# Kernel optimization log

Hardware: AMD Instinct MI355X
Metric: run time of the kernel (lower is better)

Reference implementation:

```python
import jax, jax.numpy as jnp
import numpy as np

NUM_HEADS = 8
IN_DIM = 384
HEAD_DIM = IN_DIM // NUM_HEADS  # 48


def setup_inputs() -> dict:
    key = jax.random.key(0)
    ks = jax.random.split(key, 6)
    B, N, M, C = 4, 4096, 1024, 384
    q_x = jax.random.normal(ks[0], (B, N, C), dtype=jnp.float32)
    kv_x = jax.random.normal(ks[1], (B, M, C), dtype=jnp.float32)
    s = C ** -0.5  # fan-in style init scale
    Wq = jax.random.normal(ks[2], (C, IN_DIM), dtype=jnp.float32) * s
    Wkv = jax.random.normal(ks[3], (C, 2 * IN_DIM), dtype=jnp.float32) * s
    Wproj = jax.random.normal(ks[4], (IN_DIM, IN_DIM), dtype=jnp.float32) * (IN_DIM ** -0.5)
    bproj = jnp.zeros((IN_DIM,), dtype=jnp.float32)
    return {"q_x": q_x, "kv_x": kv_x, "Wq": Wq, "Wkv": Wkv, "Wproj": Wproj, "bproj": bproj}


def reference(q_x, kv_x, Wq, Wkv, Wproj, bproj):
    B, N, C = q_x.shape
    M = kv_x.shape[1]
    scale = HEAD_DIM ** -0.5
    # q: [B, H, N, hd]
    q = (q_x @ Wq).reshape(B, N, NUM_HEADS, HEAD_DIM).transpose(0, 2, 1, 3)
    # k, v: [B, H, M, hd]
    kv = (kv_x @ Wkv).reshape(B, M, 2, NUM_HEADS, HEAD_DIM).transpose(2, 0, 3, 1, 4)
    k, v = kv[0], kv[1]
    # attention scores [B, H, N, M]
    attn = jax.nn.softmax(jnp.einsum('bhnd,bhmd->bhnm', q, k) * scale, axis=-1)
    x = jnp.einsum('bhnm,bhmd->bhnd', attn, v)  # [B, H, N, hd]
    x = x.transpose(0, 2, 1, 3).reshape(B, N, IN_DIM)
    x = x @ Wproj + bproj
    # sr_ratio == 1 residual: add raw q projection back
    q_res = q.transpose(0, 2, 1, 3).reshape(B, N, IN_DIM)
    return q_res + x
```

## Files before the change

### kernel.cpp

```cpp
#include <hip/hip_runtime.h>
#include <hip/hip_bf16.h>
#include <math.h>

#define B_ 4
#define N_ 4096
#define M_ 1024
#define C_ 384
#define NH_ 8
#define HD_ 48

typedef float f32x4 __attribute__((ext_vector_type(4)));
typedef short bf16x8 __attribute__((ext_vector_type(8)));

__device__ __forceinline__ unsigned short f2bf(float x) {
    unsigned int u = __builtin_bit_cast(unsigned int, x);
    return (unsigned short)((u + 0x7FFFu + ((u >> 16) & 1u)) >> 16);
}
__device__ __forceinline__ unsigned short f2bf_trunc(float x) {
    return (unsigned short)(__builtin_bit_cast(unsigned int, x) >> 16);
}
__device__ __forceinline__ float fast_exp2(float x) {
#if __has_builtin(__builtin_amdgcn_exp2f)
    return __builtin_amdgcn_exp2f(x);
#else
    return exp2f(x);
#endif
}

#define QSCALE 0.20823490983597203f

__global__ __launch_bounds__(256)
void conv_act(const float* __restrict__ a, unsigned short* __restrict__ da,
              const float* __restrict__ b, unsigned short* __restrict__ db)
{
    size_t i4 = (size_t)blockIdx.x * 256 + threadIdx.x;
    const float* src; unsigned short* dst;
    if (i4 < 1572864u) { src = a; dst = da; }
    else { src = b; dst = db; i4 -= 1572864u; }
    float4 v = *(const float4*)&src[i4 * 4];
    uint2 pk;
    pk.x = (unsigned int)f2bf(v.x) | ((unsigned int)f2bf(v.y) << 16);
    pk.y = (unsigned int)f2bf(v.z) | ((unsigned int)f2bf(v.w) << 16);
    *(uint2*)&dst[i4 * 4] = pk;
}

__global__ __launch_bounds__(256)
void transpose_w3(const float* __restrict__ Wq, const float* __restrict__ Wkv,
                  const float* __restrict__ Wproj,
                  unsigned short* __restrict__ Wq_t, unsigned short* __restrict__ Wkv_t,
                  unsigned short* __restrict__ Wproj_t)
{
    __shared__ unsigned short T[64 * 72];
    const int tid = threadIdx.x;
    int bid = blockIdx.x;
    const float* W; unsigned short* Wt; int N, kt, nt;
    if (bid < 36)       { W = Wq;    Wt = Wq_t;    N = 384; kt = bid / 6;  nt = bid - kt * 6; }
    else if (bid < 108) { bid -= 36;  W = Wkv;   Wt = Wkv_t;   N = 768; kt = bid / 12; nt = bid - kt * 12; }
    else                { bid -= 108; W = Wproj; Wt = Wproj_t; N = 384; kt = bid / 6;  nt = bid - kt * 6; }
    const int k0 = kt * 64, n0 = nt * 64;

    #pragma unroll
    for (int it = 0; it < 4; ++it) {
        int k = it * 16 + (tid >> 4);
        int n4 = (tid & 15) * 4;
        float4 v = *(const float4*)&W[(size_t)(k0 + k) * N + n0 + n4];
        T[(n4 + 0) * 72 + k] = f2bf(v.x);
        T[(n4 + 1) * 72 + k] = f2bf(v.y);
        T[(n4 + 2) * 72 + k] = f2bf(v.z);
        T[(n4 + 3) * 72 + k] = f2bf(v.w);
    }
    __syncthreads();
    #pragma unroll
    for (int i = 0; i < 2; ++i) {
        int s = tid + 256 * i;
        int n = s >> 3, part = s & 7;
        *(uint4*)&Wt[(size_t)(n0 + n) * C_ + k0 + part * 8] = *(const uint4*)&T[n * 72 + part * 8];
    }
}

__global__ __launch_bounds__(256)
void gemm_bf16(const unsigned short* __restrict__ A, const unsigned short* __restrict__ Wt,
               float* __restrict__ out0,
               unsigned short* __restrict__ bf0, unsigned short* __restrict__ bf1,
               const float* __restrict__ addend, const float* __restrict__ bias,
               int mode)
{
    __shared__ unsigned short As[128 * 72];
    __shared__ unsigned short Ws[64 * 72];
    const int tid = threadIdx.x;
    const int wave = tid >> 6;
    const int lane = tid & 63;
    const int ln = lane & 15;
    const int quad = lane >> 4;
    const int row0 = blockIdx.x * 128;
    const int col0 = blockIdx.y * 64;

    f32x4 acc[2][4];
    #pragma unroll
    for (int rt = 0; rt < 2; ++rt)
        #pragma unroll
        for (int t = 0; t < 4; ++t) acc[rt][t] = (f32x4){0.f, 0.f, 0.f, 0.f};

    for (int kk = 0; kk < C_; kk += 64) {
        __syncthreads();
        #pragma unroll
        for (int i = 0; i < 4; ++i) {
            int s = tid + 256 * i;
            int r = s >> 3, part = s & 7;
            *(uint4*)&As[r * 72 + part * 8] =
                *(const uint4*)&A[(size_t)(row0 + r) * C_ + kk + part * 8];
        }
        #pragma unroll
        for (int i = 0; i < 2; ++i) {
            int s = tid + 256 * i;
            int n = s >> 3, part = s & 7;
            *(uint4*)&Ws[n * 72 + part * 8] =
                *(const uint4*)&Wt[(size_t)(col0 + n) * C_ + kk + part * 8];
        }
        __syncthreads();

        bf16x8 af[2][2];
        #pragma unroll
        for (int rt = 0; rt < 2; ++rt) {
            const unsigned short* Ap = &As[(wave * 32 + rt * 16 + ln) * 72];
            af[rt][0] = *(const bf16x8*)&Ap[quad * 8];
            af[rt][1] = *(const bf16x8*)&Ap[32 + quad * 8];
        }
        #pragma unroll
        for (int t = 0; t < 4; ++t) {
            const unsigned short* Wp = &Ws[(t * 16 + ln) * 72];
            bf16x8 b0 = *(const bf16x8*)&Wp[quad * 8];
            bf16x8 b1 = *(const bf16x8*)&Wp[32 + quad * 8];
            #pragma unroll
            for (int rt = 0; rt < 2; ++rt) {
                acc[rt][t] = __builtin_amdgcn_mfma_f32_16x16x32_bf16(af[rt][0], b0, acc[rt][t], 0, 0, 0);
                acc[rt][t] = __builtin_amdgcn_mfma_f32_16x16x32_bf16(af[rt][1], b1, acc[rt][t], 0, 0, 0);
            }
        }
    }

    #pragma unroll
    for (int rt = 0; rt < 2; ++rt) {
        #pragma unroll
        for (int t = 0; t < 4; ++t) {
            int gcol = col0 + t * 16 + ln;
            #pragma unroll
            for (int r = 0; r < 4; ++r) {
                int grow = row0 + wave * 32 + rt * 16 + quad * 4 + r;
                float v = acc[rt][t][r];
                if (mode == 0) {
                    out0[(size_t)grow * C_ + gcol] = v;
                    int b = grow >> 12, n = grow & (N_ - 1);
                    int h = gcol / HD_, d = gcol - h * HD_;
                    bf0[(((size_t)(b * NH_ + h) * N_) + n) * HD_ + d] = f2bf(v * QSCALE);
                } else if (mode == 1) {
                    int b = grow >> 10, m = grow & (M_ - 1);
                    if (gcol < C_) {
                        int h = gcol / HD_, d = gcol - h * HD_;
                        bf0[(((size_t)(b * NH_ + h) * M_) + m) * HD_ + d] = f2bf(v);
                    } else {
                        int c2 = gcol - C_;
                        int h = c2 / HD_, d = c2 - h * HD_;
                        bf1[(((size_t)(b * NH_ + h) * HD_) + d) * M_ + m] = f2bf(v);
                    }
                } else {
                    size_t idx = (size_t)grow * C_ + gcol;
                    out0[idx] = v + addend[idx] + bias[gcol];
                }
            }
        }
    }
}

__global__ __launch_bounds__(256)
void attn_mfma(const unsigned short* __restrict__ qbf,
               const unsigned short* __restrict__ kbf,
               const unsigned short* __restrict__ vbf,
               unsigned short* __restrict__ of)
{
    __shared__ unsigned short QP[64 * 72];
    __shared__ unsigned short Ks[64 * 72];
    __shared__ unsigned short Vt[64 * 72];

    const int tid = threadIdx.x;
    const int wave = tid >> 6;
    const int lane = tid & 63;
    const int ln = lane & 15;
    const int quad = lane >> 4;
    const int bh = blockIdx.y;
    const int n0 = blockIdx.x * 64;

    uint4 z4; z4.x = z4.y = z4.z = z4.w = 0u;
    for (int e = tid; e < 576; e += 256) {
        *(uint4*)&QP[e * 8] = z4;
        *(uint4*)&Ks[e * 8] = z4;
        *(uint4*)&Vt[e * 8] = z4;
    }
    __syncthreads();
    if (tid < 64) Vt[48 * 72 + tid] = 0x3F80;
    const unsigned short* qsrc = qbf + ((size_t)bh * N_ + n0) * HD_;
    for (int e = tid; e < 384; e += 256) {
        int r = e / 6, part = e - r * 6;
        *(uint4*)&QP[r * 72 + part * 8] = *(const uint4*)&qsrc[r * HD_ + part * 8];
    }
    __syncthreads();

    const unsigned short* Qw = &QP[(wave * 16 + ln) * 72];
    bf16x8 aq0 = *(const bf16x8*)&Qw[quad * 8];
    bf16x8 aq1 = *(const bf16x8*)&Qw[32 + quad * 8];

    f32x4 O[4];
    #pragma unroll
    for (int t = 0; t < 4; ++t) O[t] = (f32x4){0.f, 0.f, 0.f, 0.f};

    const unsigned short* ksrc = kbf + (size_t)bh * M_ * HD_;
    const unsigned short* vsrc = vbf + (size_t)bh * HD_ * M_;
    unsigned short* Pw = &QP[wave * 16 * 72];
    const int phys_r = (ln & 3) * 4 + (ln >> 2);
    const unsigned short* Pr = &QP[(wave * 16 + phys_r) * 72];

    for (int mt = 0; mt < M_ / 64; ++mt) {
        __syncthreads();
        const unsigned short* kp = ksrc + (size_t)mt * 64 * HD_;
        for (int e = tid; e < 384; e += 256) {
            int r = e / 6, part = e - r * 6;
            *(uint4*)&Ks[r * 72 + part * 8] = *(const uint4*)&kp[r * HD_ + part * 8];
        }
        for (int e = tid; e < 384; e += 256) {
            int d = e >> 3, part = e & 7;
            *(uint4*)&Vt[d * 72 + part * 8] =
                *(const uint4*)&vsrc[(size_t)d * M_ + mt * 64 + part * 8];
        }
        __syncthreads();

        f32x4 S[4];
        #pragma unroll
        for (int t = 0; t < 4; ++t) S[t] = (f32x4){0.f, 0.f, 0.f, 0.f};
        #pragma unroll
        for (int t = 0; t < 4; ++t) {
            const unsigned short* Kp = &Ks[(t * 16 + ln) * 72];
            bf16x8 b0 = *(const bf16x8*)&Kp[quad * 8];
            S[t] = __builtin_amdgcn_mfma_f32_16x16x32_bf16(aq0, b0, S[t], 0, 0, 0);
            bf16x8 b1 = *(const bf16x8*)&Kp[32 + quad * 8];
            S[t] = __builtin_amdgcn_mfma_f32_16x16x32_bf16(aq1, b1, S[t], 0, 0, 0);
        }

        #pragma unroll
        for (int t = 0; t < 4; ++t)
            #pragma unroll
            for (int r = 0; r < 4; ++r)
                Pw[(r * 4 + quad) * 72 + t * 16 + ln] = f2bf_trunc(fast_exp2(S[t][r]));

        bf16x8 pa0 = *(const bf16x8*)&Pr[quad * 8];
        bf16x8 pa1 = *(const bf16x8*)&Pr[32 + quad * 8];
        #pragma unroll
        for (int ot = 0; ot < 4; ++ot) {
            const unsigned short* Vp = &Vt[(ot * 16 + ln) * 72];
            bf16x8 b0 = *(const bf16x8*)&Vp[quad * 8];
            O[ot] = __builtin_amdgcn_mfma_f32_16x16x32_bf16(pa0, b0, O[ot], 0, 0, 0);
            bf16x8 b1 = *(const bf16x8*)&Vp[32 + quad * 8];
            O[ot] = __builtin_amdgcn_mfma_f32_16x16x32_bf16(pa1, b1, O[ot], 0, 0, 0);
        }
    }

    const int b = bh >> 3, h = bh & 7;
    float inv[4];
    #pragma unroll
    for (int r = 0; r < 4; ++r)
        inv[r] = 1.0f / __shfl(O[3][r], lane & 48);
    #pragma unroll
    for (int ot = 0; ot < 3; ++ot) {
        int gcol = h * HD_ + ot * 16 + ln;
        #pragma unroll
        for (int r = 0; r < 4; ++r) {
            int grow = n0 + wave * 16 + quad * 4 + r;
            of[((size_t)b * N_ + grow) * C_ + gcol] = f2bf(O[ot][r] * inv[r]);
        }
    }
}

extern "C" void kernel_launch(void* const* d_in, const int* in_sizes, int n_in,
                              void* d_out, int out_size, void* d_ws, size_t ws_size,
                              hipStream_t stream) {
    const float* q_x   = (const float*)d_in[0];
    const float* kv_x  = (const float*)d_in[1];
    const float* Wq    = (const float*)d_in[2];
    const float* Wkv   = (const float*)d_in[3];
    const float* Wproj = (const float*)d_in[4];
    const float* bproj = (const float*)d_in[5];
    float* out = (float*)d_out;

    float* qf = (float*)d_ws;
    unsigned short* base = (unsigned short*)(qf + 6291456);
    unsigned short* qx_bf   = base;
    unsigned short* kvx_bf  = qx_bf  + 6291456;
    unsigned short* qbf     = kvx_bf + 1572864;
    unsigned short* kbf     = qbf    + 6291456;
    unsigned short* vbf     = kbf    + 1572864;
    unsigned short* Wq_t    = vbf    + 1572864;
    unsigned short* Wkv_t   = Wq_t   + 147456;
    unsigned short* Wproj_t = Wkv_t  + 294912;
    unsigned short* of      = qx_bf;

    dim3 blk(256);

    conv_act<<<dim3(7680), blk, 0, stream>>>(q_x, qx_bf, kv_x, kvx_bf);
    transpose_w3<<<dim3(144), blk, 0, stream>>>(Wq, Wkv, Wproj, Wq_t, Wkv_t, Wproj_t);

    gemm_bf16<<<dim3(128, 6), blk, 0, stream>>>(
        qx_bf, Wq_t, qf, qbf, nullptr, nullptr, nullptr, 0);

    gemm_bf16<<<dim3(32, 12), blk, 0, stream>>>(
        kvx_bf, Wkv_t, nullptr, kbf, vbf, nullptr, nullptr, 1);

    attn_mfma<<<dim3(64, 32), blk, 0, stream>>>(qbf, kbf, vbf, of);

    gemm_bf16<<<dim3(128, 6), blk, 0, stream>>>(
        of, Wproj_t, out, nullptr, nullptr, qf, bproj, 2);
}
```

Baseline: 208.4 us.

## Fuse activation conversion into GEMMs and restructure attention without LDS K/V staging

Removes the separate fp32-to-bf16 conversion kernel by converting activations inside the GEMM A-tile load, and stores the q residual as bf16 instead of fp32 to cut bandwidth. The attention kernel is rewritten so each wave handles 32 query rows, loading K and V fragments directly from global memory instead of staging them in shared memory with block barriers, and computing the softmax denominator via an MFMA against a ones vector. This trades barrier and LDS traffic for redundant global/L2 reads per wave and adds bf16 rounding of the residual.

```diff
diff --git a/kernel.cpp b/kernel.cpp
--- a/kernel.cpp
+++ b/kernel.cpp
@@ -19,6 +19,9 @@
 __device__ __forceinline__ unsigned short f2bf_trunc(float x) {
     return (unsigned short)(__builtin_bit_cast(unsigned int, x) >> 16);
 }
+__device__ __forceinline__ float bf2f(unsigned short x) {
+    return __builtin_bit_cast(float, (unsigned int)x << 16);
+}
 __device__ __forceinline__ float fast_exp2(float x) {
 #if __has_builtin(__builtin_amdgcn_exp2f)
     return __builtin_amdgcn_exp2f(x);
@@ -28,21 +31,6 @@
 }
 
 #define QSCALE 0.20823490983597203f
-
-__global__ __launch_bounds__(256)
-void conv_act(const float* __restrict__ a, unsigned short* __restrict__ da,
-              const float* __restrict__ b, unsigned short* __restrict__ db)
-{
-    size_t i4 = (size_t)blockIdx.x * 256 + threadIdx.x;
-    const float* src; unsigned short* dst;
-    if (i4 < 1572864u) { src = a; dst = da; }
-    else { src = b; dst = db; i4 -= 1572864u; }
-    float4 v = *(const float4*)&src[i4 * 4];
-    uint2 pk;
-    pk.x = (unsigned int)f2bf(v.x) | ((unsigned int)f2bf(v.y) << 16);
-    pk.y = (unsigned int)f2bf(v.z) | ((unsigned int)f2bf(v.w) << 16);
-    *(uint2*)&dst[i4 * 4] = pk;
-}
 
 __global__ __launch_bounds__(256)
 void transpose_w3(const float* __restrict__ Wq, const float* __restrict__ Wkv,
@@ -79,11 +67,11 @@
 }
 
 __global__ __launch_bounds__(256)
-void gemm_bf16(const unsigned short* __restrict__ A, const unsigned short* __restrict__ Wt,
+void gemm_bf16(const void* __restrict__ Av, const unsigned short* __restrict__ Wt,
                float* __restrict__ out0,
                unsigned short* __restrict__ bf0, unsigned short* __restrict__ bf1,
-               const float* __restrict__ addend, const float* __restrict__ bias,
-               int mode)
+               const unsigned short* __restrict__ addend, const float* __restrict__ bias,
+               int mode, int a_bf16)
 {
     __shared__ unsigned short As[128 * 72];
     __shared__ unsigned short Ws[64 * 72];
@@ -103,12 +91,27 @@
 
     for (int kk = 0; kk < C_; kk += 64) {
         __syncthreads();
-        #pragma unroll
-        for (int i = 0; i < 4; ++i) {
-            int s = tid + 256 * i;
-            int r = s >> 3, part = s & 7;
-            *(uint4*)&As[r * 72 + part * 8] =
-                *(const uint4*)&A[(size_t)(row0 + r) * C_ + kk + part * 8];
+        if (a_bf16) {
+            const unsigned short* A = (const unsigned short*)Av;
+            #pragma unroll
+            for (int i = 0; i < 4; ++i) {
+                int s = tid + 256 * i;
+                int r = s >> 3, part = s & 7;
+                *(uint4*)&As[r * 72 + part * 8] =
+                    *(const uint4*)&A[(size_t)(row0 + r) * C_ + kk + part * 8];
+            }
+        } else {
+            const float* A = (const float*)Av;
+            #pragma unroll
+            for (int i = 0; i < 8; ++i) {
+                int s = tid + 256 * i;
+                int r = s >> 4, k4 = (s & 15) << 2;
+                float4 v = *(const float4*)&A[(size_t)(row0 + r) * C_ + kk + k4];
+                uint2 pk;
+                pk.x = (unsigned int)f2bf(v.x) | ((unsigned int)f2bf(v.y) << 16);
+                pk.y = (unsigned int)f2bf(v.z) | ((unsigned int)f2bf(v.w) << 16);
+                *(uint2*)&As[r * 72 + k4] = pk;
+            }
         }
         #pragma unroll
         for (int i = 0; i < 2; ++i) {
@@ -149,7 +152,7 @@
                 int grow = row0 + wave * 32 + rt * 16 + quad * 4 + r;
                 float v = acc[rt][t][r];
                 if (mode == 0) {
-                    out0[(size_t)grow * C_ + gcol] = v;
+                    bf1[(size_t)grow * C_ + gcol] = f2bf(v);
                     int b = grow >> 12, n = grow & (N_ - 1);
                     int h = gcol / HD_, d = gcol - h * HD_;
                     bf0[(((size_t)(b * NH_ + h) * N_) + n) * HD_ + d] = f2bf(v * QSCALE);
@@ -165,116 +168,121 @@
                     }
                 } else {
                     size_t idx = (size_t)grow * C_ + gcol;
-                    out0[idx] = v + addend[idx] + bias[gcol];
+                    out0[idx] = v + bf2f(addend[idx]) + bias[gcol];
                 }
             }
         }
     }
 }
 
-__global__ __launch_bounds__(256)
+__global__ __launch_bounds__(256, 4)
 void attn_mfma(const unsigned short* __restrict__ qbf,
                const unsigned short* __restrict__ kbf,
                const unsigned short* __restrict__ vbf,
                unsigned short* __restrict__ of)
 {
-    __shared__ unsigned short QP[64 * 72];
-    __shared__ unsigned short Ks[64 * 72];
-    __shared__ unsigned short Vt[64 * 72];
+    __shared__ unsigned short P[4][2][16 * 72];
 
     const int tid = threadIdx.x;
     const int wave = tid >> 6;
     const int lane = tid & 63;
     const int ln = lane & 15;
     const int quad = lane >> 4;
-    const int bh = blockIdx.y;
-    const int n0 = blockIdx.x * 64;
-
-    uint4 z4; z4.x = z4.y = z4.z = z4.w = 0u;
-    for (int e = tid; e < 576; e += 256) {
-        *(uint4*)&QP[e * 8] = z4;
-        *(uint4*)&Ks[e * 8] = z4;
-        *(uint4*)&Vt[e * 8] = z4;
-    }
-    __syncthreads();
-    if (tid < 64) Vt[48 * 72 + tid] = 0x3F80;
+    const int bh = blockIdx.x;
+    const int n0 = blockIdx.y * 128 + wave * 32;
+
+    const bf16x8 zero8 = (bf16x8){0, 0, 0, 0, 0, 0, 0, 0};
+    bf16x8 ones8;
+    #pragma unroll
+    for (int i = 0; i < 8; ++i) ones8[i] = (short)0x3F80;
+
+    bf16x8 q0[2], q1[2];
     const unsigned short* qsrc = qbf + ((size_t)bh * N_ + n0) * HD_;
-    for (int e = tid; e < 384; e += 256) {
-        int r = e / 6, part = e - r * 6;
-        *(uint4*)&QP[r * 72 + part * 8] = *(const uint4*)&qsrc[r * HD_ + part * 8];
-    }
-    __syncthreads();
-
-    const unsigned short* Qw = &QP[(wave * 16 + ln) * 72];
-    bf16x8 aq0 = *(const bf16x8*)&Qw[quad * 8];
-    bf16x8 aq1 = *(const bf16x8*)&Qw[32 + quad * 8];
-
-    f32x4 O[4];
-    #pragma unroll
-    for (int t = 0; t < 4; ++t) O[t] = (f32x4){0.f, 0.f, 0.f, 0.f};
-
-    const unsigned short* ksrc = kbf + (size_t)bh * M_ * HD_;
-    const unsigned short* vsrc = vbf + (size_t)bh * HD_ * M_;
-    unsigned short* Pw = &QP[wave * 16 * 72];
+    #pragma unroll
+    for (int rt = 0; rt < 2; ++rt) {
+        const unsigned short* qp = qsrc + (size_t)(rt * 16 + ln) * HD_;
+        q0[rt] = *(const bf16x8*)(qp + quad * 8);
+        q1[rt] = *(const bf16x8*)(qp + 32 + quad * 8);
+        if (quad >= 2) q1[rt] = zero8;
+    }
+
+    f32x4 O[2][4];
+    #pragma unroll
+    for (int rt = 0; rt < 2; ++rt)
+        #pragma unroll
+        for (int t = 0; t < 4; ++t) O[rt][t] = (f32x4){0.f, 0.f, 0.f, 0.f};
+
+    const unsigned short* kb = kbf + (size_t)bh * M_ * HD_;
+    const unsigned short* vb = vbf + (size_t)bh * HD_ * M_;
+    unsigned short* Pw[2] = { &P[wave][0][0], &P[wave][1][0] };
     const int phys_r = (ln & 3) * 4 + (ln >> 2);
-    const unsigned short* Pr = &QP[(wave * 16 + phys_r) * 72];
 
     for (int mt = 0; mt < M_ / 64; ++mt) {
-        __syncthreads();
-        const unsigned short* kp = ksrc + (size_t)mt * 64 * HD_;
-        for (int e = tid; e < 384; e += 256) {
-            int r = e / 6, part = e - r * 6;
-            *(uint4*)&Ks[r * 72 + part * 8] = *(const uint4*)&kp[r * HD_ + part * 8];
-        }
-        for (int e = tid; e < 384; e += 256) {
-            int d = e >> 3, part = e & 7;
-            *(uint4*)&Vt[d * 72 + part * 8] =
-                *(const uint4*)&vsrc[(size_t)d * M_ + mt * 64 + part * 8];
-        }
-        __syncthreads();
-
-        f32x4 S[4];
-        #pragma unroll
-        for (int t = 0; t < 4; ++t) S[t] = (f32x4){0.f, 0.f, 0.f, 0.f};
+        f32x4 S[2][4];
+        #pragma unroll
+        for (int rt = 0; rt < 2; ++rt)
+            #pragma unroll
+            for (int t = 0; t < 4; ++t) S[rt][t] = (f32x4){0.f, 0.f, 0.f, 0.f};
+        const unsigned short* krow = kb + (size_t)mt * 64 * HD_;
         #pragma unroll
         for (int t = 0; t < 4; ++t) {
-            const unsigned short* Kp = &Ks[(t * 16 + ln) * 72];
-            bf16x8 b0 = *(const bf16x8*)&Kp[quad * 8];
-            S[t] = __builtin_amdgcn_mfma_f32_16x16x32_bf16(aq0, b0, S[t], 0, 0, 0);
-            bf16x8 b1 = *(const bf16x8*)&Kp[32 + quad * 8];
-            S[t] = __builtin_amdgcn_mfma_f32_16x16x32_bf16(aq1, b1, S[t], 0, 0, 0);
-        }
-
-        #pragma unroll
-        for (int t = 0; t < 4; ++t)
-            #pragma unroll
-            for (int r = 0; r < 4; ++r)
-                Pw[(r * 4 + quad) * 72 + t * 16 + ln] = f2bf_trunc(fast_exp2(S[t][r]));
-
-        bf16x8 pa0 = *(const bf16x8*)&Pr[quad * 8];
-        bf16x8 pa1 = *(const bf16x8*)&Pr[32 + quad * 8];
-        #pragma unroll
-        for (int ot = 0; ot < 4; ++ot) {
-            const unsigned short* Vp = &Vt[(ot * 16 + ln) * 72];
-            bf16x8 b0 = *(const bf16x8*)&Vp[quad * 8];
-            O[ot] = __builtin_amdgcn_mfma_f32_16x16x32_bf16(pa0, b0, O[ot], 0, 0, 0);
-            bf16x8 b1 = *(const bf16x8*)&Vp[32 + quad * 8];
-            O[ot] = __builtin_amdgcn_mfma_f32_16x16x32_bf16(pa1, b1, O[ot], 0, 0, 0);
+            const unsigned short* kp = krow + (size_t)(t * 16 + ln) * HD_;
+            bf16x8 k0 = *(const bf16x8*)(kp + quad * 8);
+            bf16x8 k1 = *(const bf16x8*)(kp + 32 + quad * 8);
+            if (quad >= 2) k1 = zero8;
+            #pragma unroll
+            for (int rt = 0; rt < 2; ++rt) {
+                S[rt][t] = __builtin_amdgcn_mfma_f32_16x16x32_bf16(q0[rt], k0, S[rt][t], 0, 0, 0);
+                S[rt][t] = __builtin_amdgcn_mfma_f32_16x16x32_bf16(q1[rt], k1, S[rt][t], 0, 0, 0);
+            }
+        }
+
+        bf16x8 p0[2], p1[2];
+        #pragma unroll
+        for (int rt = 0; rt < 2; ++rt) {
+            #pragma unroll
+            for (int t = 0; t < 4; ++t)
+                #pragma unroll
+                for (int r = 0; r < 4; ++r)
+                    Pw[rt][(r * 4 + quad) * 72 + t * 16 + ln] =
+                        f2bf_trunc(fast_exp2(S[rt][t][r]));
+            const unsigned short* Pr = Pw[rt] + phys_r * 72;
+            p0[rt] = *(const bf16x8*)(Pr + quad * 8);
+            p1[rt] = *(const bf16x8*)(Pr + 32 + quad * 8);
+        }
+
+        #pragma unroll
+        for (int ot = 0; ot < 3; ++ot) {
+            const unsigned short* vp = vb + (size_t)(ot * 16 + ln) * M_ + mt * 64;
+            bf16x8 v0 = *(const bf16x8*)(vp + quad * 8);
+            bf16x8 v1 = *(const bf16x8*)(vp + 32 + quad * 8);
+            #pragma unroll
+            for (int rt = 0; rt < 2; ++rt) {
+                O[rt][ot] = __builtin_amdgcn_mfma_f32_16x16x32_bf16(p0[rt], v0, O[rt][ot], 0, 0, 0);
+                O[rt][ot] = __builtin_amdgcn_mfma_f32_16x16x32_bf16(p1[rt], v1, O[rt][ot], 0, 0, 0);
+            }
+        }
+        #pragma unroll
+        for (int rt = 0; rt < 2; ++rt) {
+            O[rt][3] = __builtin_amdgcn_mfma_f32_16x16x32_bf16(p0[rt], ones8, O[rt][3], 0, 0, 0);
+            O[rt][3] = __builtin_amdgcn_mfma_f32_16x16x32_bf16(p1[rt], ones8, O[rt][3], 0, 0, 0);
         }
     }
 
     const int b = bh >> 3, h = bh & 7;
-    float inv[4];
-    #pragma unroll
-    for (int r = 0; r < 4; ++r)
-        inv[r] = 1.0f / __shfl(O[3][r], lane & 48);
-    #pragma unroll
-    for (int ot = 0; ot < 3; ++ot) {
-        int gcol = h * HD_ + ot * 16 + ln;
-        #pragma unroll
-        for (int r = 0; r < 4; ++r) {
-            int grow = n0 + wave * 16 + quad * 4 + r;
-            of[((size_t)b * N_ + grow) * C_ + gcol] = f2bf(O[ot][r] * inv[r]);
+    #pragma unroll
+    for (int rt = 0; rt < 2; ++rt) {
+        float inv[4];
+        #pragma unroll
+        for (int r = 0; r < 4; ++r) inv[r] = 1.0f / O[rt][3][r];
+        #pragma unroll
+        for (int ot = 0; ot < 3; ++ot) {
+            int gcol = h * HD_ + ot * 16 + ln;
+            #pragma unroll
+            for (int r = 0; r < 4; ++r) {
+                int grow = n0 + rt * 16 + quad * 4 + r;
+                of[((size_t)b * N_ + grow) * C_ + gcol] = f2bf(O[rt][ot][r] * inv[r]);
+            }
         }
     }
 }
@@ -290,31 +298,27 @@
     const float* bproj = (const float*)d_in[5];
     float* out = (float*)d_out;
 
-    float* qf = (float*)d_ws;
-    unsigned short* base = (unsigned short*)(qf + 6291456);
-    unsigned short* qx_bf   = base;
-    unsigned short* kvx_bf  = qx_bf  + 6291456;
-    unsigned short* qbf     = kvx_bf + 1572864;
-    unsigned short* kbf     = qbf    + 6291456;
-    unsigned short* vbf     = kbf    + 1572864;
-    unsigned short* Wq_t    = vbf    + 1572864;
-    unsigned short* Wkv_t   = Wq_t   + 147456;
-    unsigned short* Wproj_t = Wkv_t  + 294912;
-    unsigned short* of      = qx_bf;
+    unsigned short* qbf     = (unsigned short*)d_ws;
+    unsigned short* kbf     = qbf     + 6291456;
+    unsigned short* vbf     = kbf     + 1572864;
+    unsigned short* qres    = vbf     + 1572864;
+    unsigned short* of      = qres    + 6291456;
+    unsigned short* Wq_t    = of      + 6291456;
+    unsigned short* Wkv_t   = Wq_t    + 147456;
+    unsigned short* Wproj_t = Wkv_t   + 294912;
 
     dim3 blk(256);
 
-    conv_act<<<dim3(7680), blk, 0, stream>>>(q_x, qx_bf, kv_x, kvx_bf);
     transpose_w3<<<dim3(144), blk, 0, stream>>>(Wq, Wkv, Wproj, Wq_t, Wkv_t, Wproj_t);
 
     gemm_bf16<<<dim3(128, 6), blk, 0, stream>>>(
-        qx_bf, Wq_t, qf, qbf, nullptr, nullptr, nullptr, 0);
+        q_x, Wq_t, nullptr, qbf, qres, nullptr, nullptr, 0, 0);
 
     gemm_bf16<<<dim3(32, 12), blk, 0, stream>>>(
-        kvx_bf, Wkv_t, nullptr, kbf, vbf, nullptr, nullptr, 1);
-
-    attn_mfma<<<dim3(64, 32), blk, 0, stream>>>(qbf, kbf, vbf, of);
+        kv_x, Wkv_t, nullptr, kbf, vbf, nullptr, nullptr, 1, 0);
+
+    attn_mfma<<<dim3(32, 32), blk, 0, stream>>>(qbf, kbf, vbf, of);
 
     gemm_bf16<<<dim3(128, 6), blk, 0, stream>>>(
-        of, Wproj_t, out, nullptr, nullptr, qf, bproj, 2);
-}
+        of, Wproj_t, out, nullptr, nullptr, qres, bproj, 2, 1);
+}
```

New measurement: 225.8 us. 8.4% more time.
